# Kernel tuning notes

Hardware: AMD Instinct MI355X
Metric: run time of the kernel (lower is better)

## Reference

```python
import jax, jax.numpy as jnp
import numpy as np

LOSS_WEIGHT = 1.0


def _norm_gram(feat):
    # feat: [B, C, H, W] -> normalized channel gram [B, C, C]
    B, C, H, W = feat.shape
    F = feat.reshape(B, C, H * W)                      # [B, C, HW]
    gram = jnp.einsum('bcn,bdn->bcd', F, F)            # [B, C, C]
    n = jnp.sqrt(jnp.sum(F * F, axis=2))               # [B, C] per-channel L2 norm
    norm_M = n[:, :, None] * n[:, None, :]             # [B, C, C]
    return gram / norm_M


def setup_inputs() -> dict:
    key = jax.random.key(0)
    k1, k2 = jax.random.split(key)
    det = jax.random.normal(k1, (8, 512, 128, 128), dtype=jnp.float32)
    sr = jax.random.normal(k2, (8, 512, 128, 128), dtype=jnp.float32)
    return {"det": det, "sr": sr}


def reference(det, sr):
    sm_det = _norm_gram(det)
    sm_sr = _norm_gram(sr)
    # use_l2=True -> MSELoss (mean reduction); weighted_loss with weight=None,
    # reduction='mean' on a scalar is identity; then * loss_weight.
    loss = jnp.mean((sm_det - sm_sr) ** 2)
    return loss * LOSS_WEIGHT
```

## Files before the change

### kernel.cpp

```cpp
#include <hip/hip_runtime.h>
#include <hip/hip_bf16.h>

#define C_CH 512
#define HW 16384
#define NB 8
#define TILE 128
#define BK 32
#define NTB 4
#define NTILES 10
#define KSPLIT 8
#define KCHUNK (HW / KSPLIT)
#define KSTEPS (KCHUNK / BK)
#define NGRAM 16
#define CC (C_CH * C_CH)
#define LOSS_BLOCKS 1024
#define GRID (NGRAM * KSPLIT * NTILES)
#define PANEL_V8 (TILE * BK / 8)

typedef float f32x4 __attribute__((ext_vector_type(4)));
typedef float f32x8 __attribute__((ext_vector_type(8)));
typedef __bf16 bf16x8 __attribute__((ext_vector_type(8)));

__device__ __forceinline__ int slot_of(int R, int c) {
    return (R >> 1) * 8 + ((((R & 1) << 2) + c) ^ ((R >> 1) & 7));
}

__global__ __launch_bounds__(256, 2) void gram_kernel(const float* __restrict__ det,
                                                      const float* __restrict__ sr,
                                                      float* __restrict__ gram) {
    const int lbid = ((int)blockIdx.x & 7) * (GRID / 8) + ((int)blockIdx.x >> 3);
    const int t = lbid % NTILES;
    const int gk = lbid / NTILES;
    const int ks = gk & (KSPLIT - 1);
    const int g = gk >> 3;
    const int tensor = g >> 3, b = g & 7;

    int ti = 0, tt = t;
    while (tt >= NTB - ti) { tt -= NTB - ti; ++ti; }
    const int tj = ti + tt;
    const bool diag = (ti == tj);

    const float* F = (tensor ? sr : det) + (size_t)b * C_CH * HW;
    const float* Abase = F + (size_t)(ti * TILE) * HW + ks * KCHUNK;
    const float* Bbase = F + (size_t)(tj * TILE) * HW + ks * KCHUNK;

    __shared__ bf16x8 lds[4 * PANEL_V8];

    const int tid = threadIdx.x;
    const int lane = tid & 63;
    const int wid = tid >> 6;
    const int wr = wid >> 1, wc = wid & 1;

    int goff[2], lslot[2];
    #pragma unroll
    for (int q = 0; q < 2; ++q) {
        int c = q * 256 + tid;
        int r = c >> 2, ch = c & 3;
        goff[q] = r * HW + ch * 8;
        lslot[q] = slot_of(r, ch);
    }

    f32x8 a0[2], b0[2], a1[2], b1[2];
    auto LOAD0 = [&](int kt) {
        const int ko = kt * BK;
        #pragma unroll
        for (int q = 0; q < 2; ++q) a0[q] = *(const f32x8*)(Abase + goff[q] + ko);
        if (!diag) {
            #pragma unroll
            for (int q = 0; q < 2; ++q) b0[q] = *(const f32x8*)(Bbase + goff[q] + ko);
        }
    };
    auto LOAD1 = [&](int kt) {
        const int ko = kt * BK;
        #pragma unroll
        for (int q = 0; q < 2; ++q) a1[q] = *(const f32x8*)(Abase + goff[q] + ko);
        if (!diag) {
            #pragma unroll
            for (int q = 0; q < 2; ++q) b1[q] = *(const f32x8*)(Bbase + goff[q] + ko);
        }
    };
    auto WRITE0 = [&]() {
        bf16x8* As = lds;
        #pragma unroll
        for (int q = 0; q < 2; ++q) {
            bf16x8 h;
            #pragma unroll
            for (int i = 0; i < 8; ++i) h[i] = (__bf16)a0[q][i];
            As[lslot[q]] = h;
        }
        if (!diag) {
            bf16x8* Bs = As + PANEL_V8;
            #pragma unroll
            for (int q = 0; q < 2; ++q) {
                bf16x8 h;
                #pragma unroll
                for (int i = 0; i < 8; ++i) h[i] = (__bf16)b0[q][i];
                Bs[lslot[q]] = h;
            }
        }
    };
    auto WRITE1 = [&]() {
        bf16x8* As = lds + 2 * PANEL_V8;
        #pragma unroll
        for (int q = 0; q < 2; ++q) {
            bf16x8 h;
            #pragma unroll
            for (int i = 0; i < 8; ++i) h[i] = (__bf16)a1[q][i];
            As[lslot[q]] = h;
        }
        if (!diag) {
            bf16x8* Bs = As + PANEL_V8;
            #pragma unroll
            for (int q = 0; q < 2; ++q) {
                bf16x8 h;
                #pragma unroll
                for (int i = 0; i < 8; ++i) h[i] = (__bf16)b1[q][i];
                Bs[lslot[q]] = h;
            }
        }
    };

    f32x4 acc[4][4] = {};
    const int kg = lane >> 4;
    const int l15 = lane & 15;
    auto COMPUTE = [&](const bf16x8* As) {
        const bf16x8* Bs = diag ? As : As + PANEL_V8;
        bf16x8 af[4], bfr[4];
        #pragma unroll
        for (int m = 0; m < 4; ++m) {
            int R = wr * 64 + m * 16 + l15;
            af[m] = As[slot_of(R, kg)];
        }
        #pragma unroll
        for (int n = 0; n < 4; ++n) {
            int R = wc * 64 + n * 16 + l15;
            bfr[n] = Bs[slot_of(R, kg)];
        }
        #pragma unroll
        for (int m = 0; m < 4; ++m)
            #pragma unroll
            for (int n = 0; n < 4; ++n)
                if (!diag || (wc * 64 + n * 16 + 16 > wr * 64 + m * 16))
                    acc[m][n] = __builtin_amdgcn_mfma_f32_16x16x32_bf16(af[m], bfr[n], acc[m][n], 0, 0, 0);
    };

    LOAD0(0);
    WRITE0();
    LOAD1(1);
    __syncthreads();

    #pragma unroll 1
    for (int kt = 0; kt < KSTEPS; kt += 2) {
        if (kt + 2 < KSTEPS) LOAD0(kt + 2);
        COMPUTE(lds);
        WRITE1();
        __syncthreads();
        if (kt + 3 < KSTEPS) LOAD1(kt + 3);
        COMPUTE(lds + 2 * PANEL_V8);
        if (kt + 2 < KSTEPS) WRITE0();
        __syncthreads();
    }

    float* gout = gram + (size_t)g * CC;
    const int rb = ti * TILE + wr * 64 + (kg << 2);
    const int cb = tj * TILE + wc * 64 + l15;
    #pragma unroll
    for (int m = 0; m < 4; ++m)
        #pragma unroll
        for (int n = 0; n < 4; ++n) {
            if (diag && (wc * 64 + n * 16 + 16 <= wr * 64 + m * 16)) continue;
            #pragma unroll
            for (int j = 0; j < 4; ++j)
                atomicAdd(&gout[(size_t)(rb + m * 16 + j) * C_CH + cb + n * 16], acc[m][n][j]);
        }
}

__global__ void norm_kernel(const float* __restrict__ gram, float* __restrict__ invn) {
    const int g = blockIdx.x, c = threadIdx.x;
    float v = gram[(size_t)g * CC + (size_t)c * C_CH + c];
    invn[g * C_CH + c] = 1.0f / sqrtf(v);
}

__global__ __launch_bounds__(256) void loss_kernel(const float* __restrict__ gram,
                                                   const float* __restrict__ invn,
                                                   float* __restrict__ partials) {
    const int tid = threadIdx.x;
    float s = 0.f;
    for (int idx = blockIdx.x * 256 + tid; idx < NB * CC; idx += LOSS_BLOCKS * 256) {
        int b = idx >> 18;
        int c = (idx >> 9) & 511;
        int d = idx & 511;
        int cc = c, dd = d;
        if (dd < cc) { int tmp = cc; cc = dd; dd = tmp; }
        float gd = gram[(size_t)b * CC + (size_t)cc * C_CH + dd];
        float gs = gram[(size_t)(8 + b) * CC + (size_t)cc * C_CH + dd];
        float sd = gd * invn[b * C_CH + c] * invn[b * C_CH + d];
        float ss = gs * invn[(8 + b) * C_CH + c] * invn[(8 + b) * C_CH + d];
        float diff = sd - ss;
        s += diff * diff;
    }
    #pragma unroll
    for (int off = 32; off > 0; off >>= 1) s += __shfl_down(s, off, 64);
    __shared__ float red[4];
    if ((tid & 63) == 0) red[tid >> 6] = s;
    __syncthreads();
    if (tid == 0) partials[blockIdx.x] = red[0] + red[1] + red[2] + red[3];
}

__global__ void final_kernel(const float* __restrict__ partials, float* __restrict__ out) {
    const int tid = threadIdx.x;
    float s = 0.f;
    for (int i = tid; i < LOSS_BLOCKS; i += 256) s += partials[i];
    #pragma unroll
    for (int off = 32; off > 0; off >>= 1) s += __shfl_down(s, off, 64);
    __shared__ float red[4];
    if ((tid & 63) == 0) red[tid >> 6] = s;
    __syncthreads();
    if (tid == 0) out[0] = (red[0] + red[1] + red[2] + red[3]) * (1.0f / (float)(NB * (size_t)CC));
}

extern "C" void kernel_launch(void* const* d_in, const int* in_sizes, int n_in,
                              void* d_out, int out_size, void* d_ws, size_t ws_size,
                              hipStream_t stream) {
    const float* det = (const float*)d_in[0];
    const float* sr  = (const float*)d_in[1];
    float* gram     = (float*)d_ws;
    float* invn     = gram + (size_t)NGRAM * CC;
    float* partials = invn + NGRAM * C_CH;
    float* out      = (float*)d_out;

    hipMemsetAsync(gram, 0, (size_t)NGRAM * CC * sizeof(float), stream);
    gram_kernel<<<GRID, 256, 0, stream>>>(det, sr, gram);
    norm_kernel<<<NGRAM, C_CH, 0, stream>>>(gram, invn);
    loss_kernel<<<LOSS_BLOCKS, 256, 0, stream>>>(gram, invn, partials);
    final_kernel<<<1, 256, 0, stream>>>(partials, out);
}
```

Baseline: 253.5 us.

## Use lgkmcnt-only barriers, split f32x8 loads, raise occupancy hint to 3

Replaces __syncthreads with a custom barrier that waits only on LDS counters (lgkmcnt) before s_barrier, so in-flight global prefetches are not drained at each barrier. Global loads are split into two f32x4 loads per chunk, the second prefetch is issued before the first LDS write, and launch bounds request 3 blocks per SIMD to raise occupancy. The occupancy hint may force register spills or limits, and the custom barrier depends on the compiler inserting correct vmcnt waits before the register values are consumed.

```diff
diff --git a/kernel.cpp b/kernel.cpp
--- a/kernel.cpp
+++ b/kernel.cpp
@@ -18,14 +18,19 @@
 #define PANEL_V8 (TILE * BK / 8)
 
 typedef float f32x4 __attribute__((ext_vector_type(4)));
-typedef float f32x8 __attribute__((ext_vector_type(8)));
 typedef __bf16 bf16x8 __attribute__((ext_vector_type(8)));
+
+#define BAR()                                                       \
+    do {                                                            \
+        asm volatile("s_waitcnt lgkmcnt(0)" ::: "memory");          \
+        __builtin_amdgcn_s_barrier();                               \
+    } while (0)
 
 __device__ __forceinline__ int slot_of(int R, int c) {
     return (R >> 1) * 8 + ((((R & 1) << 2) + c) ^ ((R >> 1) & 7));
 }
 
-__global__ __launch_bounds__(256, 2) void gram_kernel(const float* __restrict__ det,
+__global__ __launch_bounds__(256, 3) void gram_kernel(const float* __restrict__ det,
                                                       const float* __restrict__ sr,
                                                       float* __restrict__ gram) {
     const int lbid = ((int)blockIdx.x & 7) * (GRID / 8) + ((int)blockIdx.x >> 3);
@@ -60,23 +65,35 @@
         lslot[q] = slot_of(r, ch);
     }
 
-    f32x8 a0[2], b0[2], a1[2], b1[2];
+    f32x4 a0[4], b0[4], a1[4], b1[4];
     auto LOAD0 = [&](int kt) {
         const int ko = kt * BK;
         #pragma unroll
-        for (int q = 0; q < 2; ++q) a0[q] = *(const f32x8*)(Abase + goff[q] + ko);
-        if (!diag) {
-            #pragma unroll
-            for (int q = 0; q < 2; ++q) b0[q] = *(const f32x8*)(Bbase + goff[q] + ko);
+        for (int q = 0; q < 2; ++q) {
+            a0[2 * q]     = *(const f32x4*)(Abase + goff[q] + ko);
+            a0[2 * q + 1] = *(const f32x4*)(Abase + goff[q] + ko + 4);
+        }
+        if (!diag) {
+            #pragma unroll
+            for (int q = 0; q < 2; ++q) {
+                b0[2 * q]     = *(const f32x4*)(Bbase + goff[q] + ko);
+                b0[2 * q + 1] = *(const f32x4*)(Bbase + goff[q] + ko + 4);
+            }
         }
     };
     auto LOAD1 = [&](int kt) {
         const int ko = kt * BK;
         #pragma unroll
-        for (int q = 0; q < 2; ++q) a1[q] = *(const f32x8*)(Abase + goff[q] + ko);
-        if (!diag) {
-            #pragma unroll
-            for (int q = 0; q < 2; ++q) b1[q] = *(const f32x8*)(Bbase + goff[q] + ko);
+        for (int q = 0; q < 2; ++q) {
+            a1[2 * q]     = *(const f32x4*)(Abase + goff[q] + ko);
+            a1[2 * q + 1] = *(const f32x4*)(Abase + goff[q] + ko + 4);
+        }
+        if (!diag) {
+            #pragma unroll
+            for (int q = 0; q < 2; ++q) {
+                b1[2 * q]     = *(const f32x4*)(Bbase + goff[q] + ko);
+                b1[2 * q + 1] = *(const f32x4*)(Bbase + goff[q] + ko + 4);
+            }
         }
     };
     auto WRITE0 = [&]() {
@@ -85,7 +102,7 @@
         for (int q = 0; q < 2; ++q) {
             bf16x8 h;
             #pragma unroll
-            for (int i = 0; i < 8; ++i) h[i] = (__bf16)a0[q][i];
+            for (int i = 0; i < 4; ++i) { h[i] = (__bf16)a0[2 * q][i]; h[4 + i] = (__bf16)a0[2 * q + 1][i]; }
             As[lslot[q]] = h;
         }
         if (!diag) {
@@ -94,7 +111,7 @@
             for (int q = 0; q < 2; ++q) {
                 bf16x8 h;
                 #pragma unroll
-                for (int i = 0; i < 8; ++i) h[i] = (__bf16)b0[q][i];
+                for (int i = 0; i < 4; ++i) { h[i] = (__bf16)b0[2 * q][i]; h[4 + i] = (__bf16)b0[2 * q + 1][i]; }
                 Bs[lslot[q]] = h;
             }
         }
@@ -105,7 +122,7 @@
         for (int q = 0; q < 2; ++q) {
             bf16x8 h;
             #pragma unroll
-            for (int i = 0; i < 8; ++i) h[i] = (__bf16)a1[q][i];
+            for (int i = 0; i < 4; ++i) { h[i] = (__bf16)a1[2 * q][i]; h[4 + i] = (__bf16)a1[2 * q + 1][i]; }
             As[lslot[q]] = h;
         }
         if (!diag) {
@@ -114,7 +131,7 @@
             for (int q = 0; q < 2; ++q) {
                 bf16x8 h;
                 #pragma unroll
-                for (int i = 0; i < 8; ++i) h[i] = (__bf16)b1[q][i];
+                for (int i = 0; i < 4; ++i) { h[i] = (__bf16)b1[2 * q][i]; h[4 + i] = (__bf16)b1[2 * q + 1][i]; }
                 Bs[lslot[q]] = h;
             }
         }
@@ -145,20 +162,20 @@
     };
 
     LOAD0(0);
+    LOAD1(1);
     WRITE0();
-    LOAD1(1);
-    __syncthreads();
+    BAR();
 
     #pragma unroll 1
     for (int kt = 0; kt < KSTEPS; kt += 2) {
         if (kt + 2 < KSTEPS) LOAD0(kt + 2);
         COMPUTE(lds);
         WRITE1();
-        __syncthreads();
+        BAR();
         if (kt + 3 < KSTEPS) LOAD1(kt + 3);
         COMPUTE(lds + 2 * PANEL_V8);
         if (kt + 2 < KSTEPS) WRITE0();
-        __syncthreads();
+        BAR();
     }
 
     float* gout = gram + (size_t)g * CC;
```

Result: slower. 597.6 us (+135.8%).
